# Kernel tuning notes

Hardware: AMD Instinct MI355X
Metric: run time of the kernel (lower is better)

Reference implementation:

```python
import jax, jax.numpy as jnp
import numpy as np

N_FINE = 400000
N_COARSE = 100000
E_POOL = 1200000
E_CONV = 1600000
E_UNPOOL = 1200000
C = 64


def setup_inputs() -> dict:
    key = jax.random.key(0)
    ks = jax.random.split(key, 16)
    s = 1.0 / np.sqrt(C)
    return {
        "x": jax.random.normal(ks[0], (N_FINE, C), dtype=jnp.float32),
        "W1_root": jax.random.normal(ks[1], (C, C), dtype=jnp.float32) * s,
        "W1_nb": jax.random.normal(ks[2], (C, C), dtype=jnp.float32) * s,
        "b1": jax.random.normal(ks[3], (C,), dtype=jnp.float32) * s,
        "W2_root": jax.random.normal(ks[4], (C, C), dtype=jnp.float32) * s,
        "W2_nb": jax.random.normal(ks[5], (C, C), dtype=jnp.float32) * s,
        "b2": jax.random.normal(ks[6], (C,), dtype=jnp.float32) * s,
        "pool_src": jax.random.randint(ks[7], (E_POOL,), 0, N_FINE),
        "pool_dst": jax.random.randint(ks[8], (E_POOL,), 0, N_COARSE),
        "pool_attr": jax.random.uniform(ks[9], (E_POOL, 1), dtype=jnp.float32),
        "conv_src": jax.random.randint(ks[10], (E_CONV,), 0, N_COARSE),
        "conv_dst": jax.random.randint(ks[11], (E_CONV,), 0, N_COARSE),
        "conv_attr": jax.random.uniform(ks[12], (E_CONV, 1), dtype=jnp.float32),
        "unpool_src": jax.random.randint(ks[13], (E_UNPOOL,), 0, N_COARSE),
        "unpool_dst": jax.random.randint(ks[14], (E_UNPOOL,), 0, N_FINE),
        "unpool_attr": jax.random.uniform(ks[15], (E_UNPOOL, 1), dtype=jnp.float32),
        "n_coarse": N_COARSE,
        "n_fine": N_FINE,
    }


def reference(x, W1_root, W1_nb, b1, W2_root, W2_nb, b2,
              pool_src, pool_dst, pool_attr,
              conv_src, conv_dst, conv_attr,
              unpool_src, unpool_dst, unpool_attr,
              n_coarse, n_fine):
    # CustomPoolingAdd: weighted scatter-add fine -> coarse
    xc = jax.ops.segment_sum(x[pool_src] * pool_attr, pool_dst,
                             num_segments=n_coarse)  # [n_coarse, C]

    # CustomGraphConvPointPoint: h_i' = W_root h_i + b + sum_j w_ij * (W_nb h_j)
    def conv(h, Wr, Wn, b):
        msg = jax.ops.segment_sum((h @ Wn)[conv_src] * conv_attr, conv_dst,
                                  num_segments=n_coarse)
        return h @ Wr + msg + b

    h = conv(xc, W1_root, W1_nb, b1)
    h = conv(h, W2_root, W2_nb, b2)

    # CustomUnpooling: weighted scatter-add coarse -> fine
    out = jax.ops.segment_sum(h[unpool_src] * unpool_attr, unpool_dst,
                              num_segments=n_fine)  # [n_fine, C]
    return out
```

## Files before the change

### kernel.cpp

```cpp
#include <hip/hip_runtime.h>


#define NCH 64


__global__ __launch_bounds__(256) void hist_rank_kernel(
    const int* __restrict__ dst, int* __restrict__ cnt, int* __restrict__ rank,
    int nE) {
  int t = blockIdx.x * blockDim.x + threadIdx.x;
  int e0 = t * 4;
  if (e0 + 3 < nE) {
    int4 d = *(const int4*)(dst + e0);
    int r0 = atomicAdd(&cnt[d.x], 1);
    int r1 = atomicAdd(&cnt[d.y], 1);
    int r2 = atomicAdd(&cnt[d.z], 1);
    int r3 = atomicAdd(&cnt[d.w], 1);
    *(int4*)(rank + e0) = make_int4(r0, r1, r2, r3);
  } else {
    for (int e = e0; e < nE; ++e) rank[e] = atomicAdd(&cnt[dst[e]], 1);
  }
}

static __device__ __forceinline__ int wave_incl_scan(int v, int lane) {
#pragma unroll
  for (int off = 1; off < 64; off <<= 1) {
    int t = __shfl_up(v, off, 64);
    if (lane >= off) v += t;
  }
  return v;
}

__global__ __launch_bounds__(256) void scan_reduce(const int* __restrict__ cnt,
                                                   int* __restrict__ bsums,
                                                   int n) {
  int base = blockIdx.x * 2048 + threadIdx.x * 8;
  int s = 0;
#pragma unroll
  for (int j = 0; j < 8; ++j) {
    int idx = base + j;
    s += (idx < n) ? cnt[idx] : 0;
  }
  int lane = threadIdx.x & 63;
  int w = threadIdx.x >> 6;
#pragma unroll
  for (int off = 32; off; off >>= 1) s += __shfl_xor(s, off, 64);
  __shared__ int ws_[4];
  if (lane == 0) ws_[w] = s;
  __syncthreads();
  if (threadIdx.x == 0) bsums[blockIdx.x] = ws_[0] + ws_[1] + ws_[2] + ws_[3];
}

__global__ void scan_bsums(int* __restrict__ bs, int nB) {
  int lane = threadIdx.x;
  int carry = 0;
  for (int base = 0; base < nB; base += 64) {
    int i = base + lane;
    int orig = (i < nB) ? bs[i] : 0;
    int v = wave_incl_scan(orig, lane);
    if (i < nB) bs[i] = v - orig + carry;
    carry += __shfl(v, 63, 64);
  }
}

__global__ __launch_bounds__(256) void scan_final(int* __restrict__ cnt_rowptr,
                                                  const int* __restrict__ bsums,
                                                  int n) {
  int base = blockIdx.x * 2048 + threadIdx.x * 8;
  int v[8];
  int s = 0;
#pragma unroll
  for (int j = 0; j < 8; ++j) {
    int idx = base + j;
    v[j] = (idx < n) ? cnt_rowptr[idx] : 0;
    s += v[j];
  }
  int lane = threadIdx.x & 63;
  int w = threadIdx.x >> 6;
  int inc = wave_incl_scan(s, lane);
  __shared__ int wsum[4];
  if (lane == 63) wsum[w] = inc;
  __syncthreads();
  int woff = 0;
  for (int ww = 0; ww < w; ++ww) woff += wsum[ww];
  int excl = inc - s + woff + bsums[blockIdx.x];
#pragma unroll
  for (int j = 0; j < 8; ++j) {
    int idx = base + j;
    if (idx <= n) cnt_rowptr[idx] = excl;
    excl += v[j];
  }
}

__global__ __launch_bounds__(256) void place_kernel(
    const int* __restrict__ src, const int* __restrict__ dst,
    const float* __restrict__ attr, const int* __restrict__ rp,
    const int* __restrict__ rank, int2* __restrict__ payload, int nE) {
  int t = blockIdx.x * blockDim.x + threadIdx.x;
  int e0 = t * 4;
  if (e0 + 3 < nE) {
    int4 s = *(const int4*)(src + e0);
    int4 d = *(const int4*)(dst + e0);
    float4 a = *(const float4*)(attr + e0);
    int4 r = *(const int4*)(rank + e0);
    payload[rp[d.x] + r.x] = make_int2(s.x, __float_as_int(a.x));
    payload[rp[d.y] + r.y] = make_int2(s.y, __float_as_int(a.y));
    payload[rp[d.z] + r.z] = make_int2(s.z, __float_as_int(a.z));
    payload[rp[d.w] + r.w] = make_int2(s.w, __float_as_int(a.w));
  } else {
    for (int e = e0; e < nE; ++e)
      payload[rp[dst[e]] + rank[e]] =
          make_int2(src[e], __float_as_int(attr[e]));
  }
}

__global__ __launch_bounds__(256) void gather4_kernel(
    const float* __restrict__ in, const int* __restrict__ rowptr,
    const int2* __restrict__ payload, float* __restrict__ out, int nDst) {
  const int wid = (blockIdx.x * blockDim.x + threadIdx.x) >> 6;
  const int lane = threadIdx.x & 63;
  if (wid >= nDst) return;
  const int beg = rowptr[wid];
  const int end = rowptr[wid + 1];
  const int g = lane >> 4;
  const int cq = (lane & 15) * 4;

  float4 acc = make_float4(0.f, 0.f, 0.f, 0.f);
  const int2 z = make_int2(0, 0);
  for (int jb = beg; jb < end; jb += 16) {
    const int j0 = jb + g, j1 = j0 + 4, j2 = j0 + 8, j3 = j0 + 12;
    int2 p0 = (j0 < end) ? payload[j0] : z;
    int2 p1 = (j1 < end) ? payload[j1] : z;
    int2 p2 = (j2 < end) ? payload[j2] : z;
    int2 p3 = (j3 < end) ? payload[j3] : z;
    float4 v0 = *(const float4*)(in + (size_t)p0.x * NCH + cq);
    float4 v1 = *(const float4*)(in + (size_t)p1.x * NCH + cq);
    float4 v2 = *(const float4*)(in + (size_t)p2.x * NCH + cq);
    float4 v3 = *(const float4*)(in + (size_t)p3.x * NCH + cq);
    const float a0 = __int_as_float(p0.y), a1 = __int_as_float(p1.y);
    const float a2 = __int_as_float(p2.y), a3 = __int_as_float(p3.y);
    acc.x = __builtin_fmaf(v0.x, a0, acc.x);
    acc.y = __builtin_fmaf(v0.y, a0, acc.y);
    acc.z = __builtin_fmaf(v0.z, a0, acc.z);
    acc.w = __builtin_fmaf(v0.w, a0, acc.w);
    acc.x = __builtin_fmaf(v1.x, a1, acc.x);
    acc.y = __builtin_fmaf(v1.y, a1, acc.y);
    acc.z = __builtin_fmaf(v1.z, a1, acc.z);
    acc.w = __builtin_fmaf(v1.w, a1, acc.w);
    acc.x = __builtin_fmaf(v2.x, a2, acc.x);
    acc.y = __builtin_fmaf(v2.y, a2, acc.y);
    acc.z = __builtin_fmaf(v2.z, a2, acc.z);
    acc.w = __builtin_fmaf(v2.w, a2, acc.w);
    acc.x = __builtin_fmaf(v3.x, a3, acc.x);
    acc.y = __builtin_fmaf(v3.y, a3, acc.y);
    acc.z = __builtin_fmaf(v3.z, a3, acc.z);
    acc.w = __builtin_fmaf(v3.w, a3, acc.w);
  }
#pragma unroll
  for (int off = 16; off <= 32; off <<= 1) {
    acc.x += __shfl_xor(acc.x, off, 64);
    acc.y += __shfl_xor(acc.y, off, 64);
    acc.z += __shfl_xor(acc.z, off, 64);
    acc.w += __shfl_xor(acc.w, off, 64);
  }
  if (g == 0) *(float4*)(out + (size_t)wid * NCH + cq) = acc;
}

__global__ __launch_bounds__(256) void node_gemm2_kernel(
    const float* __restrict__ h, const float* __restrict__ g,
    const float* __restrict__ Wr, const float* __restrict__ Wn,
    const float* __restrict__ bias, float* __restrict__ out, int n) {
  const int lane = threadIdx.x & 63;

  float wr[64], wn[64];
#pragma unroll
  for (int k = 0; k < 64; ++k) {
    wr[k] = Wr[k * NCH + lane];
    wn[k] = Wn[k * NCH + lane];
  }
  const float bv = bias[lane];

  const int wave = (blockIdx.x * blockDim.x + threadIdx.x) >> 6;
  const int nwaves = (gridDim.x * blockDim.x) >> 6;

  for (int i = wave; i < n; i += nwaves) {
    float hv = h[(size_t)i * NCH + lane];
    float gv = g[(size_t)i * NCH + lane];
    float acc = bv;
#pragma unroll
    for (int k = 0; k < 64; ++k) {
      acc = __builtin_fmaf(
          __uint_as_float(__builtin_amdgcn_readlane(__float_as_uint(hv), k)),
          wr[k], acc);
      acc = __builtin_fmaf(
          __uint_as_float(__builtin_amdgcn_readlane(__float_as_uint(gv), k)),
          wn[k], acc);
    }
    out[(size_t)i * NCH + lane] = acc;
  }
}

extern "C" void kernel_launch(void* const* d_in, const int* in_sizes, int n_in,
                              void* d_out, int out_size, void* d_ws,
                              size_t ws_size, hipStream_t stream) {
  const float* x = (const float*)d_in[0];
  const float* W1r = (const float*)d_in[1];
  const float* W1n = (const float*)d_in[2];
  const float* b1 = (const float*)d_in[3];
  const float* W2r = (const float*)d_in[4];
  const float* W2n = (const float*)d_in[5];
  const float* b2 = (const float*)d_in[6];
  const int* pool_src = (const int*)d_in[7];
  const int* pool_dst = (const int*)d_in[8];
  const float* pool_attr = (const float*)d_in[9];
  const int* conv_src = (const int*)d_in[10];
  const int* conv_dst = (const int*)d_in[11];
  const float* conv_attr = (const float*)d_in[12];
  const int* unpool_src = (const int*)d_in[13];
  const int* unpool_dst = (const int*)d_in[14];
  const float* unpool_attr = (const float*)d_in[15];

  const int Ep = in_sizes[7];
  const int Ec = in_sizes[10];
  const int Eu = in_sizes[13];
  const int NC = 100000;
  const int NF = 400000;

  const size_t MiB = 1024u * 1024u;

  char* ws = (char*)d_ws;
  float* bufA = (float*)ws;
  int* up_rp = (int*)(ws + 26 * MiB);
  int2* up_pl = (int2*)(ws + 28 * MiB);

  char* ob = (char*)d_out;
  float* bufB = (float*)ob;
  float* bufC = (float*)(ob + 26 * MiB);
  int* cv_rp = (int*)(ob + 52 * MiB);
  int2* cv_pl = (int2*)(ob + 53 * MiB);
  int* pl_rp = (int*)(ob + 66 * MiB);
  int2* pl_pl = (int2*)(ob + 67 * MiB);
  int* rank = (int*)(ob + 77 * MiB);
  int* bsums = (int*)(ob + 84 * MiB);

  const dim3 blk(256);

  auto build_csr = [&](const int* srcA, const int* dstA, const float* attrA,
                       int nE, int nDst, int* rp, int2* pl) {
    int nB = (nDst + 1 + 2047) / 2048;
    int nT4 = (nE + 3) / 4;
    hipMemsetAsync(rp, 0, (size_t)(nDst + 1) * sizeof(int), stream);
    hist_rank_kernel<<<dim3((nT4 + 255) / 256), blk, 0, stream>>>(dstA, rp,
                                                                  rank, nE);
    scan_reduce<<<dim3(nB), blk, 0, stream>>>(rp, bsums, nDst);
    scan_bsums<<<dim3(1), dim3(64), 0, stream>>>(bsums, nB);
    scan_final<<<dim3(nB), blk, 0, stream>>>(rp, bsums, nDst);
    place_kernel<<<dim3((nT4 + 255) / 256), blk, 0, stream>>>(
        srcA, dstA, attrA, rp, rank, pl, nE);
  };

  build_csr(pool_src, pool_dst, pool_attr, Ep, NC, pl_rp, pl_pl);
  build_csr(conv_src, conv_dst, conv_attr, Ec, NC, cv_rp, cv_pl);
  build_csr(unpool_src, unpool_dst, unpool_attr, Eu, NF, up_rp, up_pl);

  const int gemm_grid = 2048;
  const dim3 gNC((NC + 3) / 4), gNF((NF + 3) / 4);

  gather4_kernel<<<gNC, blk, 0, stream>>>(x, pl_rp, pl_pl, bufA, NC);

  gather4_kernel<<<gNC, blk, 0, stream>>>(bufA, cv_rp, cv_pl, bufB, NC);
  node_gemm2_kernel<<<dim3(gemm_grid), blk, 0, stream>>>(bufA, bufB, W1r, W1n,
                                                         b1, bufC, NC);

  gather4_kernel<<<gNC, blk, 0, stream>>>(bufC, cv_rp, cv_pl, bufB, NC);
  node_gemm2_kernel<<<dim3(gemm_grid), blk, 0, stream>>>(bufC, bufB, W2r, W2n,
                                                         b2, bufA, NC);

  gather4_kernel<<<gNF, blk, 0, stream>>>(bufA, up_rp, up_pl, (float*)d_out,
                                          NF);
}
```

Before: 876.9 us.

## Batch CSR builds across three edge sets and fuse conv gather with node GEMM

The three CSR construction pipelines (histogram, scan, placement) now run as single batched launches, with each block picking its edge set from its block index. This replaces fifteen launches with five and lets the three graphs share each launch, so the GPU stays fuller. Each conv layer's neighbour gather is fused into the node GEMM kernel, so the aggregated message stays in registers and is broadcast with readlane instead of going through a global buffer. The cost is that the fused kernel holds 128 weight registers while also gathering, which may lower occupancy and latency hiding for the irregular loads.

```diff
diff --git a/kernel.cpp b/kernel.cpp
--- a/kernel.cpp
+++ b/kernel.cpp
@@ -3,19 +3,31 @@
 
 #define NCH 64
 
-
-__global__ __launch_bounds__(256) void hist_rank_kernel(
-    const int* __restrict__ dst, int* __restrict__ cnt, int* __restrict__ rank,
-    int nE) {
-  int t = blockIdx.x * blockDim.x + threadIdx.x;
-  int e0 = t * 4;
+__global__ __launch_bounds__(256) void hist3_kernel(
+    const int* __restrict__ d0, int* __restrict__ c0, int* __restrict__ r0,
+    int n0, int b0, const int* __restrict__ d1, int* __restrict__ c1,
+    int* __restrict__ r1, int n1, int b1, const int* __restrict__ d2,
+    int* __restrict__ c2, int* __restrict__ r2, int n2) {
+  int bid = blockIdx.x;
+  const int* dst;
+  int* cnt;
+  int* rank;
+  int nE;
+  if (bid < b0) {
+    dst = d0; cnt = c0; rank = r0; nE = n0;
+  } else if (bid < b0 + b1) {
+    bid -= b0; dst = d1; cnt = c1; rank = r1; nE = n1;
+  } else {
+    bid -= b0 + b1; dst = d2; cnt = c2; rank = r2; nE = n2;
+  }
+  int e0 = (bid * 256 + (int)threadIdx.x) * 4;
   if (e0 + 3 < nE) {
     int4 d = *(const int4*)(dst + e0);
-    int r0 = atomicAdd(&cnt[d.x], 1);
-    int r1 = atomicAdd(&cnt[d.y], 1);
-    int r2 = atomicAdd(&cnt[d.z], 1);
-    int r3 = atomicAdd(&cnt[d.w], 1);
-    *(int4*)(rank + e0) = make_int4(r0, r1, r2, r3);
+    int r0v = atomicAdd(&cnt[d.x], 1);
+    int r1v = atomicAdd(&cnt[d.y], 1);
+    int r2v = atomicAdd(&cnt[d.z], 1);
+    int r3v = atomicAdd(&cnt[d.w], 1);
+    *(int4*)(rank + e0) = make_int4(r0v, r1v, r2v, r3v);
   } else {
     for (int e = e0; e < nE; ++e) rank[e] = atomicAdd(&cnt[dst[e]], 1);
   }
@@ -30,10 +42,22 @@
   return v;
 }
 
-__global__ __launch_bounds__(256) void scan_reduce(const int* __restrict__ cnt,
-                                                   int* __restrict__ bsums,
-                                                   int n) {
-  int base = blockIdx.x * 2048 + threadIdx.x * 8;
+__global__ __launch_bounds__(256) void scan_reduce3(
+    const int* __restrict__ a0, int* __restrict__ s0, int n0, int b0,
+    const int* __restrict__ a1, int* __restrict__ s1, int n1, int b1,
+    const int* __restrict__ a2, int* __restrict__ s2, int n2) {
+  int bid = blockIdx.x;
+  const int* cnt;
+  int* bsums;
+  int n;
+  if (bid < b0) {
+    cnt = a0; bsums = s0; n = n0;
+  } else if (bid < b0 + b1) {
+    bid -= b0; cnt = a1; bsums = s1; n = n1;
+  } else {
+    bid -= b0 + b1; cnt = a2; bsums = s2; n = n2;
+  }
+  int base = bid * 2048 + threadIdx.x * 8;
   int s = 0;
 #pragma unroll
   for (int j = 0; j < 8; ++j) {
@@ -47,10 +71,13 @@
   __shared__ int ws_[4];
   if (lane == 0) ws_[w] = s;
   __syncthreads();
-  if (threadIdx.x == 0) bsums[blockIdx.x] = ws_[0] + ws_[1] + ws_[2] + ws_[3];
-}
-
-__global__ void scan_bsums(int* __restrict__ bs, int nB) {
+  if (threadIdx.x == 0) bsums[bid] = ws_[0] + ws_[1] + ws_[2] + ws_[3];
+}
+
+__global__ void scan_bsums3(int* __restrict__ s0, int b0, int* __restrict__ s1,
+                            int b1, int* __restrict__ s2, int b2) {
+  int* bs = (blockIdx.x == 0) ? s0 : (blockIdx.x == 1) ? s1 : s2;
+  int nB = (blockIdx.x == 0) ? b0 : (blockIdx.x == 1) ? b1 : b2;
   int lane = threadIdx.x;
   int carry = 0;
   for (int base = 0; base < nB; base += 64) {
@@ -62,10 +89,22 @@
   }
 }
 
-__global__ __launch_bounds__(256) void scan_final(int* __restrict__ cnt_rowptr,
-                                                  const int* __restrict__ bsums,
-                                                  int n) {
-  int base = blockIdx.x * 2048 + threadIdx.x * 8;
+__global__ __launch_bounds__(256) void scan_final3(
+    int* __restrict__ a0, const int* __restrict__ s0, int n0, int b0,
+    int* __restrict__ a1, const int* __restrict__ s1, int n1, int b1,
+    int* __restrict__ a2, const int* __restrict__ s2, int n2) {
+  int bid = blockIdx.x;
+  int* cnt_rowptr;
+  const int* bsums;
+  int n;
+  if (bid < b0) {
+    cnt_rowptr = a0; bsums = s0; n = n0;
+  } else if (bid < b0 + b1) {
+    bid -= b0; cnt_rowptr = a1; bsums = s1; n = n1;
+  } else {
+    bid -= b0 + b1; cnt_rowptr = a2; bsums = s2; n = n2;
+  }
+  int base = bid * 2048 + threadIdx.x * 8;
   int v[8];
   int s = 0;
 #pragma unroll
@@ -82,7 +121,7 @@
   __syncthreads();
   int woff = 0;
   for (int ww = 0; ww < w; ++ww) woff += wsum[ww];
-  int excl = inc - s + woff + bsums[blockIdx.x];
+  int excl = inc - s + woff + bsums[bid];
 #pragma unroll
   for (int j = 0; j < 8; ++j) {
     int idx = base + j;
@@ -91,12 +130,34 @@
   }
 }
 
-__global__ __launch_bounds__(256) void place_kernel(
-    const int* __restrict__ src, const int* __restrict__ dst,
-    const float* __restrict__ attr, const int* __restrict__ rp,
-    const int* __restrict__ rank, int2* __restrict__ payload, int nE) {
-  int t = blockIdx.x * blockDim.x + threadIdx.x;
-  int e0 = t * 4;
+__global__ __launch_bounds__(256) void place3_kernel(
+    const int* __restrict__ sA0, const int* __restrict__ dA0,
+    const float* __restrict__ aA0, const int* __restrict__ rpA0,
+    const int* __restrict__ rkA0, int2* __restrict__ plA0, int n0, int b0,
+    const int* __restrict__ sA1, const int* __restrict__ dA1,
+    const float* __restrict__ aA1, const int* __restrict__ rpA1,
+    const int* __restrict__ rkA1, int2* __restrict__ plA1, int n1, int b1,
+    const int* __restrict__ sA2, const int* __restrict__ dA2,
+    const float* __restrict__ aA2, const int* __restrict__ rpA2,
+    const int* __restrict__ rkA2, int2* __restrict__ plA2, int n2) {
+  int bid = blockIdx.x;
+  const int *src, *dst, *rp, *rank;
+  const float* attr;
+  int2* payload;
+  int nE;
+  if (bid < b0) {
+    src = sA0; dst = dA0; attr = aA0; rp = rpA0; rank = rkA0; payload = plA0;
+    nE = n0;
+  } else if (bid < b0 + b1) {
+    bid -= b0;
+    src = sA1; dst = dA1; attr = aA1; rp = rpA1; rank = rkA1; payload = plA1;
+    nE = n1;
+  } else {
+    bid -= b0 + b1;
+    src = sA2; dst = dA2; attr = aA2; rp = rpA2; rank = rkA2; payload = plA2;
+    nE = n2;
+  }
+  int e0 = (bid * 256 + (int)threadIdx.x) * 4;
   if (e0 + 3 < nE) {
     int4 s = *(const int4*)(src + e0);
     int4 d = *(const int4*)(dst + e0);
@@ -108,12 +169,12 @@
     payload[rp[d.w] + r.w] = make_int2(s.w, __float_as_int(a.w));
   } else {
     for (int e = e0; e < nE; ++e)
-      payload[rp[dst[e]] + rank[e]] =
-          make_int2(src[e], __float_as_int(attr[e]));
-  }
-}
-
-__global__ __launch_bounds__(256) void gather4_kernel(
+      payload[rp[dst[e]] + rank[e]] = make_int2(src[e], __float_as_int(attr[e]));
+  }
+}
+
+template <int TAG>
+__global__ __launch_bounds__(256) void gather4_t(
     const float* __restrict__ in, const int* __restrict__ rowptr,
     const int2* __restrict__ payload, float* __restrict__ out, int nDst) {
   const int wid = (blockIdx.x * blockDim.x + threadIdx.x) >> 6;
@@ -165,10 +226,12 @@
   if (g == 0) *(float4*)(out + (size_t)wid * NCH + cq) = acc;
 }
 
-__global__ __launch_bounds__(256) void node_gemm2_kernel(
-    const float* __restrict__ h, const float* __restrict__ g,
-    const float* __restrict__ Wr, const float* __restrict__ Wn,
-    const float* __restrict__ bias, float* __restrict__ out, int n) {
+template <int TAG>
+__global__ __launch_bounds__(256) void conv_fused_t(
+    const float* __restrict__ h, const int* __restrict__ rowptr,
+    const int2* __restrict__ payload, const float* __restrict__ Wr,
+    const float* __restrict__ Wn, const float* __restrict__ bias,
+    float* __restrict__ out, int n) {
   const int lane = threadIdx.x & 63;
 
   float wr[64], wn[64];
@@ -179,23 +242,69 @@
   }
   const float bv = bias[lane];
 
+  const int g = lane >> 4;
+  const int cq = (lane & 15) * 4;
   const int wave = (blockIdx.x * blockDim.x + threadIdx.x) >> 6;
   const int nwaves = (gridDim.x * blockDim.x) >> 6;
+  const int2 z = make_int2(0, 0);
 
   for (int i = wave; i < n; i += nwaves) {
+    const int beg = rowptr[i];
+    const int end = rowptr[i + 1];
+    float4 acc = make_float4(0.f, 0.f, 0.f, 0.f);
+    for (int jb = beg; jb < end; jb += 16) {
+      const int j0 = jb + g, j1 = j0 + 4, j2 = j0 + 8, j3 = j0 + 12;
+      int2 p0 = (j0 < end) ? payload[j0] : z;
+      int2 p1 = (j1 < end) ? payload[j1] : z;
+      int2 p2 = (j2 < end) ? payload[j2] : z;
+      int2 p3 = (j3 < end) ? payload[j3] : z;
+      float4 v0 = *(const float4*)(h + (size_t)p0.x * NCH + cq);
+      float4 v1 = *(const float4*)(h + (size_t)p1.x * NCH + cq);
+      float4 v2 = *(const float4*)(h + (size_t)p2.x * NCH + cq);
+      float4 v3 = *(const float4*)(h + (size_t)p3.x * NCH + cq);
+      const float a0 = __int_as_float(p0.y), a1 = __int_as_float(p1.y);
+      const float a2 = __int_as_float(p2.y), a3 = __int_as_float(p3.y);
+      acc.x = __builtin_fmaf(v0.x, a0, acc.x);
+      acc.y = __builtin_fmaf(v0.y, a0, acc.y);
+      acc.z = __builtin_fmaf(v0.z, a0, acc.z);
+      acc.w = __builtin_fmaf(v0.w, a0, acc.w);
+      acc.x = __builtin_fmaf(v1.x, a1, acc.x);
+      acc.y = __builtin_fmaf(v1.y, a1, acc.y);
+      acc.z = __builtin_fmaf(v1.z, a1, acc.z);
+      acc.w = __builtin_fmaf(v1.w, a1, acc.w);
+      acc.x = __builtin_fmaf(v2.x, a2, acc.x);
+      acc.y = __builtin_fmaf(v2.y, a2, acc.y);
+      acc.z = __builtin_fmaf(v2.z, a2, acc.z);
+      acc.w = __builtin_fmaf(v2.w, a2, acc.w);
+      acc.x = __builtin_fmaf(v3.x, a3, acc.x);
+      acc.y = __builtin_fmaf(v3.y, a3, acc.y);
+      acc.z = __builtin_fmaf(v3.z, a3, acc.z);
+      acc.w = __builtin_fmaf(v3.w, a3, acc.w);
+    }
+#pragma unroll
+    for (int off = 16; off <= 32; off <<= 1) {
+      acc.x += __shfl_xor(acc.x, off, 64);
+      acc.y += __shfl_xor(acc.y, off, 64);
+      acc.z += __shfl_xor(acc.z, off, 64);
+      acc.w += __shfl_xor(acc.w, off, 64);
+    }
     float hv = h[(size_t)i * NCH + lane];
-    float gv = g[(size_t)i * NCH + lane];
-    float acc = bv;
+    float o = bv;
 #pragma unroll
     for (int k = 0; k < 64; ++k) {
-      acc = __builtin_fmaf(
+      const int q = k >> 2;
+      const float gcomp = ((k & 3) == 0)   ? acc.x
+                          : ((k & 3) == 1) ? acc.y
+                          : ((k & 3) == 2) ? acc.z
+                                           : acc.w;
+      o = __builtin_fmaf(
           __uint_as_float(__builtin_amdgcn_readlane(__float_as_uint(hv), k)),
-          wr[k], acc);
-      acc = __builtin_fmaf(
-          __uint_as_float(__builtin_amdgcn_readlane(__float_as_uint(gv), k)),
-          wn[k], acc);
+          wr[k], o);
+      o = __builtin_fmaf(
+          __uint_as_float(__builtin_amdgcn_readlane(__float_as_uint(gcomp), q)),
+          wn[k], o);
     }
-    out[(size_t)i * NCH + lane] = acc;
+    out[(size_t)i * NCH + lane] = o;
   }
 }
 
@@ -233,48 +342,52 @@
   int2* up_pl = (int2*)(ws + 28 * MiB);
 
   char* ob = (char*)d_out;
-  float* bufB = (float*)ob;
-  float* bufC = (float*)(ob + 26 * MiB);
-  int* cv_rp = (int*)(ob + 52 * MiB);
-  int2* cv_pl = (int2*)(ob + 53 * MiB);
-  int* pl_rp = (int*)(ob + 66 * MiB);
-  int2* pl_pl = (int2*)(ob + 67 * MiB);
-  int* rank = (int*)(ob + 77 * MiB);
-  int* bsums = (int*)(ob + 84 * MiB);
+  float* bufC = (float*)ob;
+  int* cv_rp = (int*)(ob + 26 * MiB);
+  int* pl_rp = (int*)(ob + 26 * MiB + 512 * 1024);
+  int2* cv_pl = (int2*)(ob + 27 * MiB);
+  int2* pl_pl = (int2*)(ob + 40 * MiB);
+  int* rank_p = (int*)(ob + 50 * MiB);
+  int* rank_c = (int*)(ob + 55 * MiB);
+  int* rank_u = (int*)(ob + 62 * MiB);
+  int* bs_p = (int*)(ob + 67 * MiB);
+  int* bs_c = bs_p + 256;
+  int* bs_u = bs_c + 256;
 
   const dim3 blk(256);
 
-  auto build_csr = [&](const int* srcA, const int* dstA, const float* attrA,
-                       int nE, int nDst, int* rp, int2* pl) {
-    int nB = (nDst + 1 + 2047) / 2048;
-    int nT4 = (nE + 3) / 4;
-    hipMemsetAsync(rp, 0, (size_t)(nDst + 1) * sizeof(int), stream);
-    hist_rank_kernel<<<dim3((nT4 + 255) / 256), blk, 0, stream>>>(dstA, rp,
-                                                                  rank, nE);
-    scan_reduce<<<dim3(nB), blk, 0, stream>>>(rp, bsums, nDst);
-    scan_bsums<<<dim3(1), dim3(64), 0, stream>>>(bsums, nB);
-    scan_final<<<dim3(nB), blk, 0, stream>>>(rp, bsums, nDst);
-    place_kernel<<<dim3((nT4 + 255) / 256), blk, 0, stream>>>(
-        srcA, dstA, attrA, rp, rank, pl, nE);
-  };
-
-  build_csr(pool_src, pool_dst, pool_attr, Ep, NC, pl_rp, pl_pl);
-  build_csr(conv_src, conv_dst, conv_attr, Ec, NC, cv_rp, cv_pl);
-  build_csr(unpool_src, unpool_dst, unpool_attr, Eu, NF, up_rp, up_pl);
-
-  const int gemm_grid = 2048;
+  auto eb = [](int nE) { return ((nE + 3) / 4 + 255) / 256; };
+  const int hb_p = eb(Ep), hb_c = eb(Ec), hb_u = eb(Eu);
+  auto sb = [](int n) { return (n + 2047) / 2048; };
+  const int sb_p = sb(NC), sb_c = sb(NC), sb_u = sb(NF);
+
+  hipMemsetAsync(cv_rp, 0, 512 * 1024 + (size_t)(NC + 1) * sizeof(int), stream);
+  hipMemsetAsync(up_rp, 0, (size_t)(NF + 1) * sizeof(int), stream);
+
+  hist3_kernel<<<dim3(hb_p + hb_c + hb_u), blk, 0, stream>>>(
+      pool_dst, pl_rp, rank_p, Ep, hb_p, conv_dst, cv_rp, rank_c, Ec, hb_c,
+      unpool_dst, up_rp, rank_u, Eu);
+  scan_reduce3<<<dim3(sb_p + sb_c + sb_u), blk, 0, stream>>>(
+      pl_rp, bs_p, NC, sb_p, cv_rp, bs_c, NC, sb_c, up_rp, bs_u, NF);
+  scan_bsums3<<<dim3(3), dim3(64), 0, stream>>>(bs_p, sb_p, bs_c, sb_c, bs_u,
+                                                sb_u);
+  scan_final3<<<dim3(sb_p + sb_c + sb_u), blk, 0, stream>>>(
+      pl_rp, bs_p, NC, sb_p, cv_rp, bs_c, NC, sb_c, up_rp, bs_u, NF);
+  place3_kernel<<<dim3(hb_p + hb_c + hb_u), blk, 0, stream>>>(
+      pool_src, pool_dst, pool_attr, pl_rp, rank_p, pl_pl, Ep, hb_p, conv_src,
+      conv_dst, conv_attr, cv_rp, rank_c, cv_pl, Ec, hb_c, unpool_src,
+      unpool_dst, unpool_attr, up_rp, rank_u, up_pl, Eu);
+
+  const int conv_grid = 2048;
   const dim3 gNC((NC + 3) / 4), gNF((NF + 3) / 4);
 
-  gather4_kernel<<<gNC, blk, 0, stream>>>(x, pl_rp, pl_pl, bufA, NC);
-
-  gather4_kernel<<<gNC, blk, 0, stream>>>(bufA, cv_rp, cv_pl, bufB, NC);
-  node_gemm2_kernel<<<dim3(gemm_grid), blk, 0, stream>>>(bufA, bufB, W1r, W1n,
-                                                         b1, bufC, NC);
-
-  gather4_kernel<<<gNC, blk, 0, stream>>>(bufC, cv_rp, cv_pl, bufB, NC);
-  node_gemm2_kernel<<<dim3(gemm_grid), blk, 0, stream>>>(bufC, bufB, W2r, W2n,
-                                                         b2, bufA, NC);
-
-  gather4_kernel<<<gNF, blk, 0, stream>>>(bufA, up_rp, up_pl, (float*)d_out,
-                                          NF);
-}
+  gather4_t<0><<<gNC, blk, 0, stream>>>(x, pl_rp, pl_pl, bufA, NC);
+
+  conv_fused_t<0><<<dim3(conv_grid), blk, 0, stream>>>(bufA, cv_rp, cv_pl, W1r,
+                                                       W1n, b1, bufC, NC);
+
+  conv_fused_t<1><<<dim3(conv_grid), blk, 0, stream>>>(bufC, cv_rp, cv_pl, W2r,
+                                                       W2n, b2, bufA, NC);
+
+  gather4_t<1><<<gNF, blk, 0, stream>>>(bufA, up_rp, up_pl, (float*)d_out, NF);
+}
```

Result: slower. 928.9 us (+5.9%).
